# Kernel optimization log

Hardware: AMD Instinct MI355X
Metric: run time of the kernel (lower is better)

## Reference

```python
import jax, jax.numpy as jnp
import numpy as np
from jax import lax

BS, L, H = 8, 2048, 1024
NH, HD = 16, 64


def setup_inputs() -> dict:
    key = jax.random.key(0)
    ks = jax.random.split(key, 4)
    s = 1.0 / np.sqrt(H)
    xav = np.sqrt(2.0 / (NH + HD))  # xavier_normal_ for ReadingHead (fan_in=HD? torch uses dims (NH,HD))
    return {
        "hidden_states": jax.random.normal(ks[0], (BS, L, H), jnp.float32),
        "K1_w": jax.random.normal(ks[1], (H, NH * HD), jnp.float32) * s,
        "K1_b": jnp.zeros((NH * HD,), jnp.float32),
        "V1_w": jax.random.normal(ks[2], (H, NH * HD), jnp.float32) * s,
        "V1_b": jnp.zeros((NH * HD,), jnp.float32),
        "bidirection_weight": jnp.full((1, 1, NH, 1, 4), 0.25, jnp.float32),
        "ReadingHead": jax.random.normal(ks[3], (NH, HD), jnp.float32) * xav,
    }


def _nearest_valid_maps(valid, L):
    # valid: [bs, L, nh] bool. Returns fm, bm: [bs, L, 2, nh] int32, matching the
    # original sequential torch loop (including its use of len_index = L-1-j for the
    # backward map's slot 0).
    bs, _, nh = valid.shape
    mask_t = jnp.moveaxis(valid, 1, 0)  # [L, bs, nh]

    def step(carry, x):
        a, b = carry
        m, v = x
        nb = jnp.where(m, a, b)
        na = jnp.where(m, v, a)
        return (na, nb), (na, nb)

    zero = jnp.zeros((bs, nh), jnp.int32)
    idx_fwd = jnp.arange(1, L, dtype=jnp.int32)
    _, (fa, fb) = lax.scan(step, (zero, zero), (mask_t[1:], idx_fwd))
    fa = jnp.concatenate([zero[None], fa], axis=0)  # [L, bs, nh]
    fb = jnp.concatenate([zero[None], fb], axis=0)

    last = jnp.full((bs, nh), L - 1, jnp.int32)
    # backward loop stores len_index = L-1-j at position j when valid
    vals_bwd = (L - 1) - jnp.arange(L - 1, dtype=jnp.int32)
    _, (ba, bb) = lax.scan(step, (last, last), (mask_t[: L - 1], vals_bwd), reverse=True)
    ba = jnp.concatenate([ba, last[None]], axis=0)
    bb = jnp.concatenate([bb, last[None]], axis=0)

    fm = jnp.stack([fa, fb], axis=2).transpose(1, 0, 2, 3)  # [bs, L, 2, nh]
    bm = jnp.stack([ba, bb], axis=2).transpose(1, 0, 2, 3)
    return fm, bm


def reference(hidden_states, K1_w, K1_b, V1_w, V1_b, bidirection_weight, ReadingHead):
    bs, length, _ = hidden_states.shape
    nh, hd = ReadingHead.shape
    K1 = jax.nn.relu(hidden_states @ K1_w + K1_b).reshape(bs, length, nh, hd)
    V1 = jax.nn.relu(hidden_states @ V1_w + V1_b).reshape(bs, length, nh, hd)
    dots = jnp.einsum('blnh,nh->bln', K1, ReadingHead)
    valid = dots > 0.5
    fm, bm = _nearest_valid_maps(valid, length)
    # gather V along sequence dim with the two nearest-valid maps
    Vf = jnp.take_along_axis(V1, fm.reshape(bs, 2 * length, nh, 1), axis=1)
    Vf = Vf.reshape(bs, length, 2, nh, hd)
    Vb = jnp.take_along_axis(V1, bm.reshape(bs, 2 * length, nh, 1), axis=1)
    Vb = Vb.reshape(bs, length, 2, nh, hd)
    # [bs, L, 4, nh, hd] -> [bs, L, nh, hd, 4], weighted sum over the 4 registers
    new_states = jnp.concatenate([Vf, Vb], axis=2).transpose(0, 1, 3, 4, 2) * bidirection_weight
    context = new_states.sum(axis=-1).reshape(bs, length, nh * hd)
    return context
```

## Files before the change

kernel.cpp:

```cpp
#include <hip/hip_runtime.h>
#include <hip/hip_bf16.h>
#include <cstdint>

#define BS 8
#define SEQ 2048
#define HDIM 1024
#define NH 16
#define HD 64
#define M_ROWS (BS * SEQ)
#define N_COLS (2 * HDIM)
#define KDIM HDIM

#define DELTA 0.025f
#define FLAG_CAP 32768

#define OFF_A      ((size_t)0)
#define OFF_BT     ((size_t)33554432)
#define OFF_FCNT   ((size_t)37748736)
#define OFF_FLIST  ((size_t)37748800)
#define OFF_BIAS   ((size_t)37879872)
#define OFF_CVH    ((size_t)41943040)
#define OFF_VALID  ((size_t)75497472)
#define OFF_MAPS   ((size_t)75759616)

typedef __attribute__((ext_vector_type(8))) __bf16 bf16x8;
typedef __attribute__((ext_vector_type(4))) float f32x4;

__device__ __forceinline__ unsigned short f2bf(float f) {
    unsigned int x = __builtin_bit_cast(unsigned int, f);
    unsigned int r = x + 0x7fffu + ((x >> 16) & 1u);
    return (unsigned short)(r >> 16);
}
__device__ __forceinline__ float bf2f(unsigned short u) {
    return __builtin_bit_cast(float, (unsigned int)u << 16);
}

__device__ __forceinline__ void g2l16(const void* gp, void* lp) {
    __builtin_amdgcn_global_load_lds(
        (__attribute__((address_space(1))) void*)(void*)gp,
        (__attribute__((address_space(3))) void*)lp, 16, 0, 0);
}

__global__ __launch_bounds__(256) void prep_kernel(const float4* __restrict__ hs4,
                                                   ushort4* __restrict__ Abf4,
                                                   const float* __restrict__ K1w,
                                                   const float* __restrict__ V1w,
                                                   unsigned short* __restrict__ Bt,
                                                   const float* __restrict__ K1b,
                                                   const float* __restrict__ V1b,
                                                   float* __restrict__ bias,
                                                   int* __restrict__ fcnt) {
    __shared__ float tile[32][33];
    const int blk = blockIdx.x;
    const int t = threadIdx.x;
    if (blk < 16384) {
        int i = blk * 256 + t;
        float4 v = hs4[i];
        ushort4 o;
        o.x = f2bf(v.x); o.y = f2bf(v.y); o.z = f2bf(v.z); o.w = f2bf(v.w);
        Abf4[i] = o;
    } else if (blk < 18432) {
        int lb = blk - 16384;
        int z = lb >> 10;
        int tk = (lb >> 5) & 31;
        int tn = lb & 31;
        const float* W = z ? V1w : K1w;
        int r = t >> 3;
        int c4 = (t & 7) * 4;
        const float4 v = *(const float4*)&W[(size_t)(tk * 32 + r) * 1024 + tn * 32 + c4];
        tile[r][c4 + 0] = v.x; tile[r][c4 + 1] = v.y;
        tile[r][c4 + 2] = v.z; tile[r][c4 + 3] = v.w;
        __syncthreads();
        int n = tn * 32 + r;
        int k = tk * 32 + c4;
        ushort4 o;
        o.x = f2bf(tile[c4 + 0][r]); o.y = f2bf(tile[c4 + 1][r]);
        o.z = f2bf(tile[c4 + 2][r]); o.w = f2bf(tile[c4 + 3][r]);
        *(ushort4*)&Bt[((size_t)z * 1024 + n) * 1024 + k] = o;
    } else {
        int i = (blk - 18432) * 256 + t;
        bias[i] = (i < 1024) ? K1b[i] : V1b[i - 1024];
        if (i == 0) *fcnt = 0;
    }
}

__global__ __launch_bounds__(512, 2) void gemm_kernel(const unsigned short* __restrict__ Abf,
                                                      const unsigned short* __restrict__ Btbf,
                                                      const float* __restrict__ bias,
                                                      const float* __restrict__ RH,
                                                      unsigned short* __restrict__ CVh,
                                                      unsigned char* __restrict__ valid,
                                                      int* __restrict__ fcnt,
                                                      int* __restrict__ flist) {
    constexpr int K = KDIM;
    __shared__ unsigned short As[2][256 * 64];
    __shared__ unsigned short Bs[2][256 * 64];
    const int t = threadIdx.x;
    const int wave = t >> 6, lane = t & 63;
    const int wm = wave >> 2, wn = wave & 3;
    const int l16 = lane & 15, quad = lane >> 4;
    const int sw = l16 & 7;

    const int wgid = blockIdx.y * 8 + blockIdx.x;
    const int swz = (wgid & 7) * 64 + (wgid >> 3);
    const int m0 = (swz >> 3) * 256, n0 = (swz & 7) * 256;

    f32x4 zero4 = {0.f, 0.f, 0.f, 0.f};
    f32x4 acc[8][4];
#pragma unroll
    for (int i = 0; i < 8; i++)
#pragma unroll
        for (int j = 0; j < 4; j++) acc[i][j] = zero4;

    const int rr = t >> 3;
    const int gsw = (t ^ rr) & 7;
    const unsigned short* gA = Abf + (size_t)(m0 + rr) * K + gsw * 8;
    const unsigned short* gB = Btbf + (size_t)(n0 + rr) * K + gsw * 8;
    char* lA = (char*)As + (size_t)wave * 1024;
    char* lB = (char*)Bs + (size_t)wave * 1024;

    auto stA = [&](int buf, int i, int kn) {
        g2l16(gA + (size_t)i * 64 * K + kn, lA + buf * 32768 + i * 8192);
    };
    auto stB = [&](int buf, int i, int kn) {
        g2l16(gB + (size_t)i * 64 * K + kn, lB + buf * 32768 + i * 8192);
    };

    auto quad4 = [&](int buf, int mh, int kk4) {
        const unsigned short* Ab = As[buf];
        const unsigned short* Bb = Bs[buf];
        const int g = (((kk4 + quad) ^ sw) << 3);
        bf16x8 af[4], bfr[4];
#pragma unroll
        for (int mt = 0; mt < 4; mt++)
            af[mt] = *(const bf16x8*)&Ab[(wm * 128 + mh * 64 + mt * 16 + l16) * 64 + g];
#pragma unroll
        for (int nt = 0; nt < 4; nt++)
            bfr[nt] = *(const bf16x8*)&Bb[(wn * 64 + nt * 16 + l16) * 64 + g];
        __builtin_amdgcn_s_setprio(1);
#pragma unroll
        for (int mt = 0; mt < 4; mt++)
#pragma unroll
            for (int nt = 0; nt < 4; nt++)
                acc[mh * 4 + mt][nt] =
                    __builtin_amdgcn_mfma_f32_16x16x32_bf16(af[mt], bfr[nt], acc[mh * 4 + mt][nt], 0, 0, 0);
        __builtin_amdgcn_s_setprio(0);
    };

#define VW4 asm volatile("s_waitcnt vmcnt(4)" ::: "memory")
#define BARR __builtin_amdgcn_s_barrier()

    stB(0, 0, 0); stB(0, 1, 0); stB(0, 2, 0); stB(0, 3, 0);
    stA(0, 0, 0); stA(0, 2, 0); stA(0, 1, 0); stA(0, 3, 0);

#pragma unroll 1
    for (int tp = 0; tp < 8; ++tp) {
        const int ka = tp * 128 + 64;
        const int kb = (tp == 7) ? 960 : tp * 128 + 128;
        stB(1, 0, ka); stB(1, 1, ka); VW4; BARR; quad4(0, 0, 0);
        stB(1, 2, ka); stB(1, 3, ka); VW4; BARR; quad4(0, 1, 0);
        stA(1, 0, ka); stA(1, 2, ka); VW4; BARR; quad4(0, 0, 4);
        stA(1, 1, ka); stA(1, 3, ka); VW4; BARR; quad4(0, 1, 4);
        BARR;
        stB(0, 0, kb); stB(0, 1, kb); VW4; BARR; quad4(1, 0, 0);
        stB(0, 2, kb); stB(0, 3, kb); VW4; BARR; quad4(1, 1, 0);
        stA(0, 0, kb); stA(0, 2, kb); VW4; BARR; quad4(1, 0, 4);
        stA(0, 1, kb); stA(0, 3, kb); VW4; BARR; quad4(1, 1, 4);
        BARR;
    }
    asm volatile("s_waitcnt vmcnt(0)" ::: "memory");
#undef VW4
#undef BARR

    if (n0 < HDIM) {
        const int n = (n0 >> 6) + wn;
        float rh[4], bv[4];
#pragma unroll
        for (int nt = 0; nt < 4; nt++) {
            int col = n * 64 + nt * 16 + l16;
            rh[nt] = RH[col];
            bv[nt] = bias[col];
        }
#pragma unroll
        for (int mt = 0; mt < 8; mt++) {
#pragma unroll
            for (int r = 0; r < 4; r++) {
                float p = 0.f;
#pragma unroll
                for (int nt = 0; nt < 4; nt++)
                    p += fmaxf(acc[mt][nt][r] + bv[nt], 0.f) * rh[nt];
#pragma unroll
                for (int s = 8; s >= 1; s >>= 1) p += __shfl_xor(p, s, 64);
                if (l16 == 0) {
                    int row = m0 + wm * 128 + mt * 16 + quad * 4 + r;
                    int b = row >> 11, l = row & (SEQ - 1);
                    valid[((size_t)b * NH + n) * SEQ + l] = (p > 0.5f) ? 1 : 0;
                    if (fabsf(p - 0.5f) < DELTA) {
                        int idx = atomicAdd(fcnt, 1);
                        if (idx < FLAG_CAP) flist[idx] = row * NH + n;
                    }
                }
            }
        }
    } else {
        const int nv0 = n0 - HDIM;
        const int head = (nv0 >> 6) + wn;
        const int b = m0 >> 11;
        const int l0 = (m0 & (SEQ - 1)) + wm * 128 + quad * 4;
        unsigned short* plane = CVh + ((size_t)(b * NH + head)) * SEQ * HD;
#pragma unroll
        for (int mt = 0; mt < 8; mt++) {
#pragma unroll
            for (int nt = 0; nt < 4; nt++) {
                const int hd = nt * 16 + l16;
                const float bvv = bias[HDIM + nv0 + wn * 64 + hd];
#pragma unroll
                for (int r = 0; r < 4; r++)
                    plane[(size_t)(l0 + mt * 16 + r) * HD + hd] = f2bf(fmaxf(acc[mt][nt][r] + bvv, 0.f));
            }
        }
    }
}

__global__ __launch_bounds__(256) void refine_kernel(const float* __restrict__ hs,
                                                     const float* __restrict__ K1w,
                                                     const float* __restrict__ K1b,
                                                     const float* __restrict__ RH,
                                                     const int* __restrict__ fcnt,
                                                     const int* __restrict__ flist,
                                                     unsigned char* __restrict__ valid) {
    int cnt = *fcnt;
    if (cnt > FLAG_CAP) cnt = FLAG_CAP;
    const int wave = threadIdx.x >> 6, d = threadIdx.x & 63;
    const int task = blockIdx.x * 4 + wave;
    if (task >= cnt) return;

    const int code = flist[task];
    const int n = code & (NH - 1);
    const int bl = code >> 4;
    const float* x = hs + (size_t)bl * HDIM;
    const float* wp = K1w + n * 64 + d;

    double acc0 = 0.0, acc1 = 0.0, acc2 = 0.0, acc3 = 0.0;
    for (int k = 0; k < KDIM; k += 32) {
        float w[32];
#pragma unroll
        for (int u = 0; u < 32; u++)
            w[u] = wp[(size_t)(k + u) * 1024];
        float4 xv[8];
#pragma unroll
        for (int u = 0; u < 8; u++)
            xv[u] = *(const float4*)(x + k + u * 4);
#pragma unroll
        for (int u = 0; u < 8; u++) {
            acc0 += (double)xv[u].x * (double)w[u * 4 + 0];
            acc1 += (double)xv[u].y * (double)w[u * 4 + 1];
            acc2 += (double)xv[u].z * (double)w[u * 4 + 2];
            acc3 += (double)xv[u].w * (double)w[u * 4 + 3];
        }
    }
    double k1 = ((acc0 + acc1) + (acc2 + acc3)) + (double)K1b[n * 64 + d];
    if (k1 < 0.0) k1 = 0.0;
    double contrib = k1 * (double)RH[n * 64 + d];
#pragma unroll
    for (int s = 32; s >= 1; s >>= 1) contrib += __shfl_xor(contrib, s, 64);
    if (d == 0) {
        int b = bl >> 11, l = bl & (SEQ - 1);
        valid[((size_t)b * NH + n) * SEQ + l] = (contrib > 0.5) ? 1 : 0;
    }
}

__global__ __launch_bounds__(64) void scan_kernel(const unsigned char* __restrict__ valid,
                                                  ushort4* __restrict__ maps) {
    int bn = blockIdx.x;
    int b = bn >> 4, n = bn & (NH - 1);
    int lane = threadIdx.x;
    __shared__ unsigned int summ[64];

    const unsigned char* vp = valid + (size_t)bn * SEQ + lane * 32;
    uint4 c0 = *(const uint4*)vp;
    uint4 c1 = *(const uint4*)(vp + 16);
    unsigned int wds[8] = {c0.x, c0.y, c0.z, c0.w, c1.x, c1.y, c1.z, c1.w};
    unsigned int mask = 0;
#pragma unroll
    for (int i = 0; i < 8; i++) {
#pragma unroll
        for (int j = 0; j < 4; j++)
            mask |= (((wds[i] >> (8 * j)) & 0xffu) ? 1u : 0u) << (i * 4 + j);
    }

    int cnt = 0, va = 0, vb = 0;
#pragma unroll
    for (int tt = 0; tt < 32; tt++) {
        if (mask & (1u << tt)) { vb = va; va = lane * 32 + tt; cnt++; }
    }
    summ[lane] = (unsigned)((cnt > 2 ? 2 : cnt) | (va << 2) | (vb << 13));
    __syncthreads();
    int a = 0, bb_ = 0;
    for (int tt = 0; tt < lane; tt++) {
        unsigned s = summ[tt];
        int c = s & 3, sva = (s >> 2) & 2047, svb = (s >> 13) & 2047;
        if (c >= 2) { a = sva; bb_ = svb; }
        else if (c == 1) { bb_ = a; a = sva; }
    }
    unsigned int fres[32];
#pragma unroll
    for (int tt = 0; tt < 32; tt++) {
        if (mask & (1u << tt)) { bb_ = a; a = lane * 32 + tt; }
        fres[tt] = (unsigned)a | ((unsigned)bb_ << 16);
    }
    __syncthreads();

    unsigned int maskb = mask;
    if (lane == 63) maskb &= ~(1u << 31);
    cnt = 0; va = 0; vb = 0;
#pragma unroll
    for (int tt = 31; tt >= 0; tt--) {
        if (maskb & (1u << tt)) { vb = va; va = (SEQ - 1) - (lane * 32 + tt); cnt++; }
    }
    summ[lane] = (unsigned)((cnt > 2 ? 2 : cnt) | (va << 2) | (vb << 13));
    __syncthreads();
    int a2 = SEQ - 1, b2 = SEQ - 1;
    for (int tt = 63; tt > lane; tt--) {
        unsigned s = summ[tt];
        int c = s & 3, sva = (s >> 2) & 2047, svb = (s >> 13) & 2047;
        if (c >= 2) { a2 = sva; b2 = svb; }
        else if (c == 1) { b2 = a2; a2 = sva; }
    }
#pragma unroll
    for (int tt = 31; tt >= 0; tt--) {
        int j = lane * 32 + tt;
        if (maskb & (1u << tt)) { b2 = a2; a2 = (SEQ - 1) - j; }
        unsigned f = fres[tt];
        maps[((size_t)b * SEQ + j) * NH + n] =
            make_ushort4((unsigned short)(f & 0xffffu), (unsigned short)(f >> 16),
                         (unsigned short)a2, (unsigned short)b2);
    }
}

__global__ __launch_bounds__(256) void gather_kernel(const unsigned short* __restrict__ CVh,
                                                     const ushort4* __restrict__ maps,
                                                     const float* __restrict__ bw,
                                                     float* __restrict__ out) {
    int bl = blockIdx.x;
    int t = threadIdx.x, n = t >> 4, q = t & 15;
    int b = bl >> 11;
    ushort4 m = maps[(size_t)bl * NH + n];
    const float4 w = *(const float4*)&bw[n * 4];
    const unsigned short* plane = CVh + ((size_t)(b * NH + n)) * SEQ * HD + q * 4;
    const ushort4 u0 = *(const ushort4*)&plane[(size_t)m.x * HD];
    const ushort4 u1 = *(const ushort4*)&plane[(size_t)m.y * HD];
    const ushort4 u2 = *(const ushort4*)&plane[(size_t)m.z * HD];
    const ushort4 u3 = *(const ushort4*)&plane[(size_t)m.w * HD];
    float4 o;
    o.x = w.x * bf2f(u0.x) + w.y * bf2f(u1.x) + w.z * bf2f(u2.x) + w.w * bf2f(u3.x);
    o.y = w.x * bf2f(u0.y) + w.y * bf2f(u1.y) + w.z * bf2f(u2.y) + w.w * bf2f(u3.y);
    o.z = w.x * bf2f(u0.z) + w.y * bf2f(u1.z) + w.z * bf2f(u2.z) + w.w * bf2f(u3.z);
    o.w = w.x * bf2f(u0.w) + w.y * bf2f(u1.w) + w.z * bf2f(u2.w) + w.w * bf2f(u3.w);
    *(float4*)&out[(size_t)bl * (NH * HD) + n * 64 + q * 4] = o;
}

extern "C" void kernel_launch(void* const* d_in, const int* in_sizes, int n_in,
                              void* d_out, int out_size, void* d_ws, size_t ws_size,
                              hipStream_t stream) {
    (void)in_sizes; (void)n_in; (void)out_size; (void)ws_size;
    const float* hs  = (const float*)d_in[0];
    const float* K1w = (const float*)d_in[1];
    const float* K1b = (const float*)d_in[2];
    const float* V1w = (const float*)d_in[3];
    const float* V1b = (const float*)d_in[4];
    const float* bw  = (const float*)d_in[5];
    const float* RH  = (const float*)d_in[6];
    float* out = (float*)d_out;
    char* ws = (char*)d_ws;

    unsigned short* Abf  = (unsigned short*)(ws + OFF_A);
    unsigned short* Btbf = (unsigned short*)(ws + OFF_BT);
    int* fcnt = (int*)(ws + OFF_FCNT);
    int* flist = (int*)(ws + OFF_FLIST);
    float* bias  = (float*)(ws + OFF_BIAS);
    unsigned short* CVh = (unsigned short*)(ws + OFF_CVH);
    unsigned char* valid = (unsigned char*)(ws + OFF_VALID);
    ushort4* maps = (ushort4*)(ws + OFF_MAPS);

    prep_kernel<<<18440, 256, 0, stream>>>((const float4*)hs, (ushort4*)Abf,
                                           K1w, V1w, Btbf, K1b, V1b, bias, fcnt);
    gemm_kernel<<<dim3(N_COLS / 256, M_ROWS / 256), 512, 0, stream>>>(
        Abf, Btbf, bias, RH, CVh, valid, fcnt, flist);
    refine_kernel<<<FLAG_CAP / 4, 256, 0, stream>>>(
        hs, K1w, K1b, RH, fcnt, flist, valid);
    scan_kernel<<<BS * NH, 64, 0, stream>>>(valid, maps);
    gather_kernel<<<BS * SEQ, 256, 0, stream>>>(CVh, maps, bw, out);
}
```

Baseline: 383.5 us.

## Restructure GEMM main loop into per-K-tile double-buffered phases with batched staging

Replaces the hand-interleaved two-tile loop, which issued one or two global-to-LDS loads before each MFMA quad, with a 16-iteration loop over 64-wide K tiles. Each iteration prefetches all of B for the next tile up front, waits and synchronises once, then runs four compute phases, issuing the A prefetch after the first phase. Each phase is bracketed by sched_barrier and two s_barriers, so the LDS fragment reads finish before the MFMAs run. The aim is simpler, more regular overlap of loads and compute. In exchange it adds more workgroup barriers per tile and coarser load batching, which could stall waves.

```diff
diff --git a/kernel.cpp b/kernel.cpp
--- a/kernel.cpp
+++ b/kernel.cpp
@@ -119,16 +119,21 @@
     char* lA = (char*)As + (size_t)wave * 1024;
     char* lB = (char*)Bs + (size_t)wave * 1024;
 
-    auto stA = [&](int buf, int i, int kn) {
-        g2l16(gA + (size_t)i * 64 * K + kn, lA + buf * 32768 + i * 8192);
+    auto stageA = [&](int buf, int kn) {
+#pragma unroll
+        for (int j = 0; j < 4; j++)
+            g2l16(gA + (size_t)j * 64 * K + kn, lA + buf * 32768 + j * 8192);
     };
-    auto stB = [&](int buf, int i, int kn) {
-        g2l16(gB + (size_t)i * 64 * K + kn, lB + buf * 32768 + i * 8192);
+    auto stageB = [&](int buf, int kn) {
+#pragma unroll
+        for (int j = 0; j < 4; j++)
+            g2l16(gB + (size_t)j * 64 * K + kn, lB + buf * 32768 + j * 8192);
     };
 
-    auto quad4 = [&](int buf, int mh, int kk4) {
-        const unsigned short* Ab = As[buf];
-        const unsigned short* Bb = Bs[buf];
+    auto phase = [&](int cur, int mh, int kk4) {
+        __builtin_amdgcn_sched_barrier(0);
+        const unsigned short* Ab = As[cur];
+        const unsigned short* Bb = Bs[cur];
         const int g = (((kk4 + quad) ^ sw) << 3);
         bf16x8 af[4], bfr[4];
 #pragma unroll
@@ -137,6 +142,7 @@
 #pragma unroll
         for (int nt = 0; nt < 4; nt++)
             bfr[nt] = *(const bf16x8*)&Bb[(wn * 64 + nt * 16 + l16) * 64 + g];
+        __builtin_amdgcn_s_barrier();
         __builtin_amdgcn_s_setprio(1);
 #pragma unroll
         for (int mt = 0; mt < 4; mt++)
@@ -145,32 +151,26 @@
                 acc[mh * 4 + mt][nt] =
                     __builtin_amdgcn_mfma_f32_16x16x32_bf16(af[mt], bfr[nt], acc[mh * 4 + mt][nt], 0, 0, 0);
         __builtin_amdgcn_s_setprio(0);
+        __builtin_amdgcn_s_barrier();
     };
 
-#define VW4 asm volatile("s_waitcnt vmcnt(4)" ::: "memory")
-#define BARR __builtin_amdgcn_s_barrier()
-
-    stB(0, 0, 0); stB(0, 1, 0); stB(0, 2, 0); stB(0, 3, 0);
-    stA(0, 0, 0); stA(0, 2, 0); stA(0, 1, 0); stA(0, 3, 0);
-
+    stageB(0, 0);
+    stageA(0, 0);
 #pragma unroll 1
-    for (int tp = 0; tp < 8; ++tp) {
-        const int ka = tp * 128 + 64;
-        const int kb = (tp == 7) ? 960 : tp * 128 + 128;
-        stB(1, 0, ka); stB(1, 1, ka); VW4; BARR; quad4(0, 0, 0);
-        stB(1, 2, ka); stB(1, 3, ka); VW4; BARR; quad4(0, 1, 0);
-        stA(1, 0, ka); stA(1, 2, ka); VW4; BARR; quad4(0, 0, 4);
-        stA(1, 1, ka); stA(1, 3, ka); VW4; BARR; quad4(0, 1, 4);
-        BARR;
-        stB(0, 0, kb); stB(0, 1, kb); VW4; BARR; quad4(1, 0, 0);
-        stB(0, 2, kb); stB(0, 3, kb); VW4; BARR; quad4(1, 1, 0);
-        stA(0, 0, kb); stA(0, 2, kb); VW4; BARR; quad4(1, 0, 4);
-        stA(0, 1, kb); stA(0, 3, kb); VW4; BARR; quad4(1, 1, 4);
-        BARR;
+    for (int tt_ = 0; tt_ < 16; ++tt_) {
+        const int cur = tt_ & 1, nxt = cur ^ 1;
+        const int kn = (tt_ == 15) ? 960 : (tt_ + 1) * 64;
+        stageB(nxt, kn);
+        asm volatile("s_waitcnt vmcnt(4)" ::: "memory");
+        __builtin_amdgcn_s_barrier();
+        asm volatile("" ::: "memory");
+        phase(cur, 0, 0);
+        stageA(nxt, kn);
+        phase(cur, 0, 4);
+        phase(cur, 1, 0);
+        phase(cur, 1, 4);
     }
     asm volatile("s_waitcnt vmcnt(0)" ::: "memory");
-#undef VW4
-#undef BARR
 
     if (n0 < HDIM) {
         const int n = (n0 >> 6) + wn;
```

New measurement: 400.8 us. 4.5% more time.
